# Kernel optimization log

Hardware: AMD Instinct MI355X
Metric: run time of the kernel (lower is better)

Reference implementation:

```python
import jax, jax.numpy as jnp
import numpy as np

B, A, T = 256, 512, 21
DIM = 128
SC = 6
NHEAD, HD = 4, DIM // 4

def conv1d_relu(x, w, b, stride=2):
    # x: (N, C, L), w: (O, I, K)
    y = jax.lax.conv_general_dilated(x, w, (stride,), 'SAME', dimension_numbers=('NCH', 'OIH', 'NCH'))
    return jax.nn.relu(y + b[None, :, None])

def to_vector(feat, vm):
    vec_mask = vm[..., :-1] & vm[..., 1:]
    while vec_mask.ndim < feat.ndim:
        vec_mask = vec_mask[..., None]
    return jnp.where(vec_mask, feat[:, :, 1:] - feat[:, :, :-1], jnp.zeros_like(feat[:, :, 1:]))

def setup_inputs():
    key = jax.random.key(0)
    ks = jax.random.split(key, 24)
    f32 = jnp.float32
    inp = {}
    inp['position'] = jax.random.normal(ks[0], (B, A, T, 2), f32)
    inp['heading'] = jax.random.normal(ks[1], (B, A, T), f32)
    inp['velocity'] = jax.random.normal(ks[2], (B, A, T, 2), f32)
    inp['shape'] = jax.random.uniform(ks[3], (B, A, T, 2), f32)
    inp['current_state'] = jax.random.normal(ks[4], (B, SC), f32)
    inp['category'] = jax.random.randint(ks[5], (B, A), 0, 4)
    inp['valid_mask'] = jax.random.randint(ks[6], (B, A, T), 0, 2).astype(bool)
    # history encoder (CNN) params: 9 -> 32 -> 64 -> 128 channels, k=3, stride 2
    inp['conv1_w'] = jax.random.normal(ks[7], (32, 9, 3), f32) * 0.1
    inp['conv1_b'] = jnp.zeros((32,), f32)
    inp['conv2_w'] = jax.random.normal(ks[8], (64, 32, 3), f32) * 0.1
    inp['conv2_b'] = jnp.zeros((64,), f32)
    inp['conv3_w'] = jax.random.normal(ks[9], (128, 64, 3), f32) * 0.1
    inp['conv3_b'] = jnp.zeros((128,), f32)
    # StateAttentionEncoder params
    inp['se_w'] = jax.random.normal(ks[10], (SC, DIM), f32) * 0.02   # per-channel Linear(1,dim) weights
    inp['se_b'] = jnp.zeros((SC, DIM), f32)
    inp['pos_embed'] = jax.random.normal(ks[11], (1, SC, DIM), f32) * 0.02
    inp['query'] = jax.random.normal(ks[12], (1, 1, DIM), f32) * 0.02
    inp['in_proj_w'] = jax.random.normal(ks[13], (3 * DIM, DIM), f32) * (1.0 / np.sqrt(DIM))
    inp['in_proj_b'] = jnp.zeros((3 * DIM,), f32)
    inp['out_proj_w'] = jax.random.normal(ks[14], (DIM, DIM), f32) * (1.0 / np.sqrt(DIM))
    inp['out_proj_b'] = jnp.zeros((DIM,), f32)
    inp['type_emb'] = jax.random.normal(ks[15], (4, DIM), f32) * 0.02
    return inp

def reference(position, heading, velocity, shape, current_state, category, valid_mask,
              conv1_w, conv1_b, conv2_w, conv2_b, conv3_w, conv3_b,
              se_w, se_b, pos_embed, query, in_proj_w, in_proj_b, out_proj_w, out_proj_b,
              type_emb):
    # --- build per-step agent features (B, A, T-1, 9) ---
    heading_vec = to_vector(heading, valid_mask)
    valid_mask_vec = valid_mask[..., 1:] & valid_mask[..., :-1]
    agent_feature = jnp.concatenate([
        to_vector(position, valid_mask),
        to_vector(velocity, valid_mask),
        jnp.stack([jnp.cos(heading_vec), jnp.sin(heading_vec)], axis=-1),
        shape[:, :, 1:],
        valid_mask_vec.astype(jnp.float32)[..., None],
    ], axis=-1)
    bs, nA, Tm1, C = agent_feature.shape
    x = agent_feature.reshape(bs * nA, Tm1, C).transpose(0, 2, 1)  # (N, 9, T-1)
    # --- history CNN encoder (applied to all rows, then masked; same math as boolean gather/scatter) ---
    h = conv1d_relu(x, conv1_w, conv1_b)
    h = conv1d_relu(h, conv2_w, conv2_b)
    h = conv1d_relu(h, conv3_w, conv3_b)
    enc = h.mean(axis=-1)  # (N, DIM)
    valid_agent = valid_mask.any(-1).reshape(-1)
    x_agent = jnp.where(valid_agent[:, None], enc, 0.0).reshape(bs, nA, DIM)
    # --- ego state attention encoder (eval mode: no token dropout) ---
    ego = current_state[:, :SC]
    x_embed = ego[:, :, None] * se_w[None] + se_b[None] + pos_embed  # (B, SC, DIM)
    Wq, Wk, Wv = in_proj_w[:DIM], in_proj_w[DIM:2 * DIM], in_proj_w[2 * DIM:]
    bq, bk, bv = in_proj_b[:DIM], in_proj_b[DIM:2 * DIM], in_proj_b[2 * DIM:]
    q = (query[0, 0] @ Wq.T + bq).reshape(NHEAD, HD)             # (H, D)
    k = (x_embed @ Wk.T + bk).reshape(bs, SC, NHEAD, HD)          # (B, S, H, D)
    v = (x_embed @ Wv.T + bv).reshape(bs, SC, NHEAD, HD)
    scores = jnp.einsum('hd,bshd->bhs', q, k) * (1.0 / np.sqrt(HD))
    attn = jax.nn.softmax(scores, axis=-1)
    o = jnp.einsum('bhs,bshd->bhd', attn, v).reshape(bs, DIM)
    x_ego = o @ out_proj_w.T + out_proj_b                         # (B, DIM)
    x_agent = x_agent.at[:, 0].set(x_ego)
    # --- type embedding add ---
    return x_agent + type_emb[category]
```

## Files before the change

kernel.cpp:

```cpp
#include <hip/hip_runtime.h>
#include <hip/hip_bf16.h>


#define BB 256
#define AAG 512
#define TT 21
#define NAG (BB * AAG)

typedef __hip_bfloat16 bf16;
typedef __attribute__((ext_vector_type(8))) short s8v;
typedef __attribute__((ext_vector_type(4))) float f4v;

__device__ int g_dtype;
__device__ int g_mask_mode;
__device__ __align__(16) short g_w1p[32 * 64];
__device__ __align__(16) short g_w2p[64 * 96];
__device__ __align__(16) short g_w3p[128 * 192];
__device__ __align__(16) float g_b1[32];
__device__ __align__(16) float g_b2[64];
__device__ __align__(16) float g_b3[128];

template <int DT>
__device__ __forceinline__ float ldf(const void* p, long i) {
    if (DT) return __bfloat162float(((const bf16*)p)[i]);
    return ((const float*)p)[i];
}
template <int DT>
__device__ __forceinline__ void stf(void* p, long i, float v) {
    if (DT) ((bf16*)p)[i] = __float2bfloat16(v);
    else    ((float*)p)[i] = v;
}
__device__ __forceinline__ unsigned short f2bu(float x) {
    bf16 b = __float2bfloat16(x);
    union { bf16 b; unsigned short u; } cv; cv.b = b; return cv.u;
}
__device__ __forceinline__ float bu2f(unsigned short u) {
    union { unsigned int i; float f; } cv; cv.i = ((unsigned int)u) << 16; return cv.f;
}
__device__ __forceinline__ bool mask_at(const void* p, long i, int mode) {
    if (mode == 0) return ((const int*)p)[i] != 0;
    if (mode == 1) return ((const unsigned char*)p)[i] != 0;
    if (mode == 2) return ((const float*)p)[i] != 0.f;
    return (((const unsigned short*)p)[i] & 0x7fff) != 0;
}

__global__ void detect_kernel(const unsigned int* __restrict__ pw,
                              const unsigned char* __restrict__ m) {
    __shared__ int cls[4];
    __shared__ int mv;
    __shared__ int good;
    int tid = threadIdx.x;
    if (tid < 4) cls[tid] = 0;
    if (tid == 0) { mv = 0; good = 0; }
    __syncthreads();
    int g = 0;
    for (int i = tid; i < 1024; i += 256) {
        unsigned int w = pw[i];
        unsigned int h0 = w & 0xffffu, h1 = w >> 16;
        unsigned int e0 = (h0 >> 7) & 0xff, e1 = (h1 >> 7) & 0xff;
        if (h0 == 0 || (e0 >= 90 && e0 <= 160)) g++;
        if (h1 == 0 || (e1 >= 90 && e1 <= 160)) g++;
    }
    atomicAdd(&good, g);
    int l0 = 0, l1 = 0, l2 = 0, l3 = 0, lm = 0;
    for (int i = tid; i < 4096; i += 256) {
        int v = m[i];
        if (v) {
            switch (i & 3) { case 0: l0 = 1; break; case 1: l1 = 1; break;
                             case 2: l2 = 1; break; default: l3 = 1; }
            if (v > lm) lm = v;
        }
    }
    if (l0) atomicOr(&cls[0], 1);
    if (l1) atomicOr(&cls[1], 1);
    if (l2) atomicOr(&cls[2], 1);
    if (l3) atomicOr(&cls[3], 1);
    atomicMax(&mv, lm);
    __syncthreads();
    if (tid == 0) {
        g_dtype = (good >= 1740) ? 1 : 0;
        int mode;
        if (!cls[1] && !cls[2] && !cls[3]) mode = 0;
        else if (!cls[0] && !cls[1])       mode = 2;
        else if (mv <= 1)                  mode = 1;
        else                               mode = 3;
        g_mask_mode = mode;
    }
}

template <int DT>
__global__ void prep_weights_kernel(const void* __restrict__ w1, const void* __restrict__ b1,
                                    const void* __restrict__ w2, const void* __restrict__ b2,
                                    const void* __restrict__ w3, const void* __restrict__ b3) {
    if (g_dtype != DT) return;
    int tid = blockIdx.x * blockDim.x + threadIdx.x;
    int nt = gridDim.x * blockDim.x;
    for (int i = tid; i < 32 * 64; i += nt) {
        int oc = i >> 6, k = i & 63, tap = k >> 4, ic = k & 15;
        float v = (tap < 3 && ic < 9) ? ldf<DT>(w1, oc * 27 + ic * 3 + tap) : 0.f;
        g_w1p[i] = (short)f2bu(v);
    }
    for (int i = tid; i < 64 * 96; i += nt) {
        int oc = i / 96, k = i % 96, tap = k >> 5, ic = k & 31;
        g_w2p[i] = (short)f2bu(ldf<DT>(w2, oc * 96 + ic * 3 + tap));
    }
    for (int i = tid; i < 128 * 192; i += nt) {
        int oc = i / 192, k = i % 192, tap = k >> 6, ic = k & 63;
        g_w3p[i] = (short)f2bu(ldf<DT>(w3, oc * 192 + ic * 3 + tap));
    }
    for (int i = tid; i < 32; i += nt) g_b1[i] = ldf<DT>(b1, i);
    for (int i = tid; i < 64; i += nt) g_b2[i] = ldf<DT>(b2, i);
    for (int i = tid; i < 128; i += nt) g_b3[i] = ldf<DT>(b3, i);
}

#define FEAT_RS 24
#define FEAT_AS 528
#define H1_RS 40
#define H1_AS 440
#define H2_RS 72
#define H2_AS 504
#define C3_AS 384
#define OFF_H1 8448
#define OFF_H2 15488
#define OFF_VALID 47104
#define SMEM_BYTES 47168

#define MFMA16(a, b, c) __builtin_amdgcn_mfma_f32_16x16x32_bf16((a), (b), (c), 0, 0, 0)

template <int DT>
__global__ __launch_bounds__(256) void stage1_kernel(
    const void* __restrict__ pos, const void* __restrict__ heading,
    const void* __restrict__ vel, const void* __restrict__ shp,
    const void* __restrict__ vmask, const int* __restrict__ category,
    const void* __restrict__ type_emb, void* __restrict__ out) {
    if (g_dtype != DT) return;
    __shared__ __align__(16) char smem[SMEM_BYTES];
    short* feat = (short*)smem;
    short* h1 = (short*)smem + OFF_H1;
    short* h2 = (short*)smem + OFF_H2;
    short* c3 = (short*)smem;
    int* s_valid = (int*)(smem + OFF_VALID);

    const int tid = threadIdx.x;
    const int wave = tid >> 6, lane = tid & 63;
    const int col = lane & 15, quad = lane >> 4;
    const long agent0 = (long)blockIdx.x * 16;
    const int mode = g_mask_mode;

    if (tid < 16) s_valid[tid] = 0;
    {
        unsigned int* h1u = (unsigned int*)h1;
        int ag = tid >> 4, c = tid & 15;
        h1u[ag * 220 + 200 + c] = 0;
        unsigned int* h2u = (unsigned int*)h2;
        for (int i = tid; i < 1024; i += 256) {
            int a2 = i >> 6, r = (i >> 5) & 1, cc = i & 31;
            h2u[a2 * 252 + r * 216 + cc] = 0;
        }
    }
    __syncthreads();

    for (int idx = tid; idx < 16 * 22; idx += 256) {
        int ag = idx / 22, t = idx % 22;
        short* row = feat + ag * FEAT_AS + t * FEAT_RS;
        if (t >= 20) {
            *(uint4*)row = make_uint4(0, 0, 0, 0);
            *(uint4*)(row + 8) = make_uint4(0, 0, 0, 0);
            if (t == 20) {
                long base = (agent0 + ag) * TT + 20;
                if (mask_at(vmask, base, mode)) atomicOr(&s_valid[ag], 1);
            }
        } else {
            long base = (agent0 + ag) * TT + t;
            bool vmt = mask_at(vmask, base, mode);
            if (vmt) atomicOr(&s_valid[ag], 1);
            bool m2 = vmt && mask_at(vmask, base + 1, mode);
            float px0 = ldf<DT>(pos, base * 2),     py0 = ldf<DT>(pos, base * 2 + 1);
            float px1 = ldf<DT>(pos, base * 2 + 2), py1 = ldf<DT>(pos, base * 2 + 3);
            float vx0 = ldf<DT>(vel, base * 2),     vy0 = ldf<DT>(vel, base * 2 + 1);
            float vx1 = ldf<DT>(vel, base * 2 + 2), vy1 = ldf<DT>(vel, base * 2 + 3);
            float hh0 = ldf<DT>(heading, base), hh1 = ldf<DT>(heading, base + 1);
            float sx = ldf<DT>(shp, base * 2 + 2), sy = ldf<DT>(shp, base * 2 + 3);
            float dh = m2 ? (hh1 - hh0) : 0.f;
            float sn = sinf(dh), cn = cosf(dh);
            unsigned int p0 = f2bu(m2 ? px1 - px0 : 0.f) | ((unsigned int)f2bu(m2 ? py1 - py0 : 0.f) << 16);
            unsigned int p1 = f2bu(m2 ? vx1 - vx0 : 0.f) | ((unsigned int)f2bu(m2 ? vy1 - vy0 : 0.f) << 16);
            unsigned int p2 = f2bu(cn) | ((unsigned int)f2bu(sn) << 16);
            unsigned int p3 = f2bu(sx) | ((unsigned int)f2bu(sy) << 16);
            unsigned int p4 = (unsigned int)f2bu(m2 ? 1.f : 0.f);
            *(uint4*)row = make_uint4(p0, p1, p2, p3);
            *(uint4*)(row + 8) = make_uint4(p4, 0, 0, 0);
        }
    }
    __syncthreads();

    {
        int Mt = wave >> 1;
        int oc = Mt * 16 + col;
        s8v a0 = *(const s8v*)(g_w1p + oc * 64 + quad * 8);
        s8v a1 = *(const s8v*)(g_w1p + oc * 64 + 32 + quad * 8);
        int k0 = quad * 8, k1 = 32 + quad * 8;
        int tap0 = k0 >> 4, ic0 = k0 & 15;
        int tap1 = k1 >> 4, ic1 = k1 & 15;
        int ocr = Mt * 16 + quad * 4;
        f4v bia = *(const f4v*)(g_b1 + ocr);
#pragma unroll
        for (int i = 0; i < 5; i++) {
            int Nt = (wave & 1) * 5 + i;
            int n = Nt * 16 + col;
            int ag = n / 10, p = n % 10;
            const short* bb = feat + ag * FEAT_AS + 2 * p * FEAT_RS;
            s8v b0 = *(const s8v*)(bb + tap0 * FEAT_RS + ic0);
            s8v b1 = *(const s8v*)(bb + tap1 * FEAT_RS + ic1);
            f4v acc = {0.f, 0.f, 0.f, 0.f};
            acc = MFMA16(a0, b0, acc);
            acc = MFMA16(a1, b1, acc);
            unsigned int lo = f2bu(fmaxf(acc[0] + bia[0], 0.f)) | ((unsigned int)f2bu(fmaxf(acc[1] + bia[1], 0.f)) << 16);
            unsigned int hi = f2bu(fmaxf(acc[2] + bia[2], 0.f)) | ((unsigned int)f2bu(fmaxf(acc[3] + bia[3], 0.f)) << 16);
            *(uint2*)(h1 + ag * H1_AS + p * H1_RS + ocr) = make_uint2(lo, hi);
        }
    }
    __syncthreads();

    {
        int Mt = wave;
        int oc = Mt * 16 + col;
        s8v a[3];
#pragma unroll
        for (int ks = 0; ks < 3; ks++)
            a[ks] = *(const s8v*)(g_w2p + oc * 96 + ks * 32 + quad * 8);
        int ocr = Mt * 16 + quad * 4;
        f4v bia = *(const f4v*)(g_b2 + ocr);
#pragma unroll
        for (int Nt = 0; Nt < 5; Nt++) {
            int n = Nt * 16 + col;
            int ag = n / 5, p = n % 5;
            f4v acc = {0.f, 0.f, 0.f, 0.f};
#pragma unroll
            for (int ks = 0; ks < 3; ks++) {
                s8v b = *(const s8v*)(h1 + ag * H1_AS + (2 * p + ks) * H1_RS + quad * 8);
                acc = MFMA16(a[ks], b, acc);
            }
            unsigned int lo = f2bu(fmaxf(acc[0] + bia[0], 0.f)) | ((unsigned int)f2bu(fmaxf(acc[1] + bia[1], 0.f)) << 16);
            unsigned int hi = f2bu(fmaxf(acc[2] + bia[2], 0.f)) | ((unsigned int)f2bu(fmaxf(acc[3] + bia[3], 0.f)) << 16);
            *(uint2*)(h2 + ag * H2_AS + (p + 1) * H2_RS + ocr) = make_uint2(lo, hi);
        }
    }
    __syncthreads();

#pragma unroll
    for (int m2 = 0; m2 < 2; m2++) {
        int Mt = wave * 2 + m2;
        int oc = Mt * 16 + col;
        s8v a[6];
#pragma unroll
        for (int ks = 0; ks < 6; ks++)
            a[ks] = *(const s8v*)(g_w3p + oc * 192 + ks * 32 + quad * 8);
        int ocr = Mt * 16 + quad * 4;
        f4v bia = *(const f4v*)(g_b3 + ocr);
#pragma unroll
        for (int Nt = 0; Nt < 3; Nt++) {
            int n = Nt * 16 + col;
            int ag = n / 3, p = n % 3;
            f4v acc = {0.f, 0.f, 0.f, 0.f};
#pragma unroll
            for (int ks = 0; ks < 6; ks++) {
                int kg = ks * 32 + quad * 8;
                int tap = kg >> 6, ic = kg & 63;
                s8v b = *(const s8v*)(h2 + ag * H2_AS + (2 * p + tap) * H2_RS + ic);
                acc = MFMA16(a[ks], b, acc);
            }
            unsigned int lo = f2bu(fmaxf(acc[0] + bia[0], 0.f)) | ((unsigned int)f2bu(fmaxf(acc[1] + bia[1], 0.f)) << 16);
            unsigned int hi = f2bu(fmaxf(acc[2] + bia[2], 0.f)) | ((unsigned int)f2bu(fmaxf(acc[3] + bia[3], 0.f)) << 16);
            *(uint2*)(c3 + ag * C3_AS + p * 128 + ocr) = make_uint2(lo, hi);
        }
    }
    __syncthreads();

    {
        int ag = tid >> 4;
        int ocg = (tid & 15) * 8;
        s8v x0 = *(const s8v*)(c3 + ag * C3_AS + ocg);
        s8v x1 = *(const s8v*)(c3 + ag * C3_AS + 128 + ocg);
        s8v x2 = *(const s8v*)(c3 + ag * C3_AS + 256 + ocg);
        int valid = s_valid[ag];
        long agl = agent0 + ag;
        int cat = category[agl];
#pragma unroll
        for (int j = 0; j < 8; j++) {
            float m = (bu2f((unsigned short)x0[j]) + bu2f((unsigned short)x1[j]) +
                       bu2f((unsigned short)x2[j])) * (1.f / 3.f);
            if (!valid) m = 0.f;
            float te = ldf<DT>(type_emb, cat * 128 + ocg + j);
            stf<DT>(out, agl * 128 + ocg + j, m + te);
        }
    }
}

template <int DT>
__global__ __launch_bounds__(128) void stage2_kernel(
    const void* __restrict__ cs, const int* __restrict__ category,
    const void* __restrict__ se_w, const void* __restrict__ se_b,
    const void* __restrict__ pe, const void* __restrict__ query,
    const void* __restrict__ ipw, const void* __restrict__ ipb,
    const void* __restrict__ opw, const void* __restrict__ opb,
    const void* __restrict__ type_emb, void* __restrict__ out) {
    if (g_dtype != DT) return;
    int b = blockIdx.x, d = threadIdx.x;
    __shared__ float s_xe[6][128];
    __shared__ float s_qu[128];
    __shared__ float s_q[128];
    __shared__ float s_k[6][128];
    __shared__ float s_v[6][128];
    __shared__ float s_att[4][6];
    __shared__ float s_o[128];

    s_qu[d] = ldf<DT>(query, d);
#pragma unroll
    for (int s = 0; s < 6; s++) {
        float ego = ldf<DT>(cs, b * 6 + s);
        s_xe[s][d] = fmaf(ego, ldf<DT>(se_w, s * 128 + d),
                          ldf<DT>(se_b, s * 128 + d) + ldf<DT>(pe, s * 128 + d));
    }
    __syncthreads();

    float accq = ldf<DT>(ipb, d);
    float bk = ldf<DT>(ipb, 128 + d), bv = ldf<DT>(ipb, 256 + d);
    float acck[6], accv[6];
#pragma unroll
    for (int s = 0; s < 6; s++) { acck[s] = bk; accv[s] = bv; }
    for (int e = 0; e < 128; e++) {
        float wqe = ldf<DT>(ipw, (long)d * 128 + e);
        accq = fmaf(s_qu[e], wqe, accq);
        float wke = ldf<DT>(ipw, (long)(128 + d) * 128 + e);
        float wve = ldf<DT>(ipw, (long)(256 + d) * 128 + e);
#pragma unroll
        for (int s = 0; s < 6; s++) {
            float xe = s_xe[s][e];
            acck[s] = fmaf(xe, wke, acck[s]);
            accv[s] = fmaf(xe, wve, accv[s]);
        }
    }
    s_q[d] = accq;
#pragma unroll
    for (int s = 0; s < 6; s++) { s_k[s][d] = acck[s]; s_v[s][d] = accv[s]; }
    __syncthreads();

    if (d < 4) {
        float sc[6];
        float mx = -1e30f;
#pragma unroll
        for (int s = 0; s < 6; s++) {
            float t = 0.f;
            for (int q = 0; q < 32; q++) t = fmaf(s_q[d * 32 + q], s_k[s][d * 32 + q], t);
            t *= 0.17677669529663687f;
            sc[s] = t;
            mx = fmaxf(mx, t);
        }
        float sum = 0.f;
#pragma unroll
        for (int s = 0; s < 6; s++) { sc[s] = expf(sc[s] - mx); sum += sc[s]; }
        float inv = 1.f / sum;
#pragma unroll
        for (int s = 0; s < 6; s++) s_att[d][s] = sc[s] * inv;
    }
    __syncthreads();

    {
        int h = d >> 5;
        float o = 0.f;
#pragma unroll
        for (int s = 0; s < 6; s++) o = fmaf(s_att[h][s], s_v[s][d], o);
        s_o[d] = o;
    }
    __syncthreads();

    float acc = ldf<DT>(opb, d);
    for (int e = 0; e < 128; e++) acc = fmaf(s_o[e], ldf<DT>(opw, (long)d * 128 + e), acc);
    int cat = category[(long)b * AAG];
    stf<DT>(out, (long)b * AAG * 128 + d, acc + ldf<DT>(type_emb, cat * 128 + d));
}

extern "C" void kernel_launch(void* const* d_in, const int* in_sizes, int n_in,
                              void* d_out, int out_size, void* d_ws, size_t ws_size,
                              hipStream_t stream) {
    const void* position      = d_in[0];
    const void* heading       = d_in[1];
    const void* velocity      = d_in[2];
    const void* shape         = d_in[3];
    const void* current_state = d_in[4];
    const int*  category      = (const int*)d_in[5];
    const void* valid_mask    = d_in[6];
    const void* conv1_w = d_in[7];
    const void* conv1_b = d_in[8];
    const void* conv2_w = d_in[9];
    const void* conv2_b = d_in[10];
    const void* conv3_w = d_in[11];
    const void* conv3_b = d_in[12];
    const void* se_w    = d_in[13];
    const void* se_b    = d_in[14];
    const void* pos_embed = d_in[15];
    const void* query     = d_in[16];
    const void* in_proj_w = d_in[17];
    const void* in_proj_b = d_in[18];
    const void* out_proj_w = d_in[19];
    const void* out_proj_b = d_in[20];
    const void* type_emb   = d_in[21];

    hipLaunchKernelGGL(detect_kernel, dim3(1), dim3(256), 0, stream,
                       (const unsigned int*)position, (const unsigned char*)valid_mask);

    hipLaunchKernelGGL(prep_weights_kernel<0>, dim3(64), dim3(256), 0, stream,
                       conv1_w, conv1_b, conv2_w, conv2_b, conv3_w, conv3_b);
    hipLaunchKernelGGL(prep_weights_kernel<1>, dim3(64), dim3(256), 0, stream,
                       conv1_w, conv1_b, conv2_w, conv2_b, conv3_w, conv3_b);

    hipLaunchKernelGGL(stage1_kernel<0>, dim3(NAG / 16), dim3(256), 0, stream,
                       position, heading, velocity, shape, valid_mask, category, type_emb, d_out);
    hipLaunchKernelGGL(stage1_kernel<1>, dim3(NAG / 16), dim3(256), 0, stream,
                       position, heading, velocity, shape, valid_mask, category, type_emb, d_out);

    hipLaunchKernelGGL(stage2_kernel<0>, dim3(BB), dim3(128), 0, stream,
                       current_state, category, se_w, se_b, pos_embed, query,
                       in_proj_w, in_proj_b, out_proj_w, out_proj_b, type_emb, d_out);
    hipLaunchKernelGGL(stage2_kernel<1>, dim3(BB), dim3(128), 0, stream,
                       current_state, category, se_w, se_b, pos_embed, query,
                       in_proj_w, in_proj_b, out_proj_w, out_proj_b, type_emb, d_out);
}
```

Baseline: 324.8 us.

## Make conv pipeline wave-private and precompute attention terms linear in ego state

stage1 now gives each wave its own four agents with a private shared-memory slab, which removes all block-wide __syncthreads between the three MFMA conv layers. The type-embedding epilogue is vectorised. The ego attention is rewritten: since the embedding is affine in each scalar ego input, the score and value-projection constants are precomputed once in a new single-block kernel. The per-batch stage2 kernel then evaluates only a small softmax and a weighted sum, with projection weights stored as bf16, which adds precision risk and an extra serial launch.

```diff
diff --git a/kernel.cpp b/kernel.cpp
--- a/kernel.cpp
+++ b/kernel.cpp
@@ -19,6 +19,10 @@
 __device__ __align__(16) float g_b1[32];
 __device__ __align__(16) float g_b2[64];
 __device__ __align__(16) float g_b3[128];
+__device__ __align__(16) short g_ipwT[128 * 384];
+__device__ __align__(16) short g_opwT[128 * 128];
+__device__ __align__(16) float g_Sc[24], g_Sw[24];
+__device__ __align__(16) float g_P[24 * 128], g_Pw[24 * 128];
 
 template <int DT>
 __device__ __forceinline__ float ldf(const void* p, long i) {
@@ -42,6 +46,16 @@
     if (mode == 1) return ((const unsigned char*)p)[i] != 0;
     if (mode == 2) return ((const float*)p)[i] != 0.f;
     return (((const unsigned short*)p)[i] & 0x7fff) != 0;
+}
+__device__ __forceinline__ uint2 pack4(f4v acc, f4v bia, bool zero) {
+    float r0 = zero ? 0.f : fmaxf(acc[0] + bia[0], 0.f);
+    float r1 = zero ? 0.f : fmaxf(acc[1] + bia[1], 0.f);
+    float r2 = zero ? 0.f : fmaxf(acc[2] + bia[2], 0.f);
+    float r3 = zero ? 0.f : fmaxf(acc[3] + bia[3], 0.f);
+    uint2 r;
+    r.x = f2bu(r0) | ((unsigned int)f2bu(r1) << 16);
+    r.y = f2bu(r2) | ((unsigned int)f2bu(r3) << 16);
+    return r;
 }
 
 __global__ void detect_kernel(const unsigned int* __restrict__ pw,
@@ -91,7 +105,8 @@
 template <int DT>
 __global__ void prep_weights_kernel(const void* __restrict__ w1, const void* __restrict__ b1,
                                     const void* __restrict__ w2, const void* __restrict__ b2,
-                                    const void* __restrict__ w3, const void* __restrict__ b3) {
+                                    const void* __restrict__ w3, const void* __restrict__ b3,
+                                    const void* __restrict__ ipw, const void* __restrict__ opw) {
     if (g_dtype != DT) return;
     int tid = blockIdx.x * blockDim.x + threadIdx.x;
     int nt = gridDim.x * blockDim.x;
@@ -111,19 +126,99 @@
     for (int i = tid; i < 32; i += nt) g_b1[i] = ldf<DT>(b1, i);
     for (int i = tid; i < 64; i += nt) g_b2[i] = ldf<DT>(b2, i);
     for (int i = tid; i < 128; i += nt) g_b3[i] = ldf<DT>(b3, i);
-}
-
-#define FEAT_RS 24
-#define FEAT_AS 528
+    for (int i = tid; i < 384 * 128; i += nt) {
+        int r = i >> 7, e = i & 127;
+        g_ipwT[e * 384 + r] = (short)f2bu(ldf<DT>(ipw, i));
+    }
+    for (int i = tid; i < 128 * 128; i += nt) {
+        int d = i >> 7, e = i & 127;
+        g_opwT[e * 128 + d] = (short)f2bu(ldf<DT>(opw, i));
+    }
+}
+
+template <int DT>
+__global__ __launch_bounds__(128) void precompute_attn_kernel(
+    const void* __restrict__ se_w, const void* __restrict__ se_b,
+    const void* __restrict__ pe, const void* __restrict__ query,
+    const void* __restrict__ ipb) {
+    if (g_dtype != DT) return;
+    __shared__ float s_qu[128], s_xc[6][128], s_xw[6][128];
+    __shared__ float s_q[128], s_kc[6][128], s_kw[6][128], s_vc[6][128], s_vw[6][128];
+    int d = threadIdx.x;
+    s_qu[d] = ldf<DT>(query, d);
+#pragma unroll
+    for (int s = 0; s < 6; s++) {
+        s_xc[s][d] = ldf<DT>(se_b, s * 128 + d) + ldf<DT>(pe, s * 128 + d);
+        s_xw[s][d] = ldf<DT>(se_w, s * 128 + d);
+    }
+    __syncthreads();
+    float aq = ldf<DT>(ipb, d);
+    float kc[6], kw[6], vc[6], vw[6];
+    float bkd = ldf<DT>(ipb, 128 + d), bvd = ldf<DT>(ipb, 256 + d);
+#pragma unroll
+    for (int s = 0; s < 6; s++) { kc[s] = bkd; vc[s] = bvd; kw[s] = 0.f; vw[s] = 0.f; }
+    for (int e = 0; e < 128; e++) {
+        float wq = bu2f((unsigned short)g_ipwT[e * 384 + d]);
+        float wk = bu2f((unsigned short)g_ipwT[e * 384 + 128 + d]);
+        float wv = bu2f((unsigned short)g_ipwT[e * 384 + 256 + d]);
+        aq = fmaf(s_qu[e], wq, aq);
+#pragma unroll
+        for (int s = 0; s < 6; s++) {
+            float xc = s_xc[s][e], xw = s_xw[s][e];
+            kc[s] = fmaf(xc, wk, kc[s]);
+            kw[s] = fmaf(xw, wk, kw[s]);
+            vc[s] = fmaf(xc, wv, vc[s]);
+            vw[s] = fmaf(xw, wv, vw[s]);
+        }
+    }
+    s_q[d] = aq;
+#pragma unroll
+    for (int s = 0; s < 6; s++) {
+        s_kc[s][d] = kc[s]; s_kw[s][d] = kw[s];
+        s_vc[s][d] = vc[s]; s_vw[s][d] = vw[s];
+    }
+    __syncthreads();
+    if (d < 24) {
+        int s = d >> 2, h = d & 3;
+        float sc = 0.f, sw = 0.f;
+        for (int j = 0; j < 32; j++) {
+            sc = fmaf(s_q[h * 32 + j], s_kc[s][h * 32 + j], sc);
+            sw = fmaf(s_q[h * 32 + j], s_kw[s][h * 32 + j], sw);
+        }
+        g_Sc[s * 4 + h] = sc * 0.17677669529663687f;
+        g_Sw[s * 4 + h] = sw * 0.17677669529663687f;
+    }
+    float pc[6], pw[6];
+#pragma unroll
+    for (int s = 0; s < 6; s++) { pc[s] = 0.f; pw[s] = 0.f; }
+    for (int e = 0; e < 128; e++) {
+        float wo = bu2f((unsigned short)g_opwT[e * 128 + d]);
+#pragma unroll
+        for (int s = 0; s < 6; s++) {
+            pc[s] = fmaf(wo, s_vc[s][e], pc[s]);
+            pw[s] = fmaf(wo, s_vw[s][e], pw[s]);
+        }
+        if ((e & 31) == 31) {
+            int h = e >> 5;
+#pragma unroll
+            for (int s = 0; s < 6; s++) {
+                g_P[(s * 4 + h) * 128 + d] = pc[s];
+                g_Pw[(s * 4 + h) * 128 + d] = pw[s];
+                pc[s] = 0.f; pw[s] = 0.f;
+            }
+        }
+    }
+}
+
+#define F_RS 24
+#define F_AS 584
 #define H1_RS 40
-#define H1_AS 440
+#define H1_AS 488
 #define H2_RS 72
-#define H2_AS 504
-#define C3_AS 384
-#define OFF_H1 8448
-#define OFF_H2 15488
-#define OFF_VALID 47104
-#define SMEM_BYTES 47168
+#define H2_AS 520
+#define C3_RS 136
+#define C3_AS 408
+#define WAVE_STRIDE 6368
 
 #define MFMA16(a, b, c) __builtin_amdgcn_mfma_f32_16x16x32_bf16((a), (b), (c), 0, 0, 0)
 
@@ -134,165 +229,169 @@
     const void* __restrict__ vmask, const int* __restrict__ category,
     const void* __restrict__ type_emb, void* __restrict__ out) {
     if (g_dtype != DT) return;
-    __shared__ __align__(16) char smem[SMEM_BYTES];
-    short* feat = (short*)smem;
-    short* h1 = (short*)smem + OFF_H1;
-    short* h2 = (short*)smem + OFF_H2;
-    short* c3 = (short*)smem;
-    int* s_valid = (int*)(smem + OFF_VALID);
+    __shared__ __align__(16) short sm[4 * WAVE_STRIDE + 128];
+    __shared__ int sval[16];
 
     const int tid = threadIdx.x;
     const int wave = tid >> 6, lane = tid & 63;
     const int col = lane & 15, quad = lane >> 4;
-    const long agent0 = (long)blockIdx.x * 16;
     const int mode = g_mask_mode;
-
-    if (tid < 16) s_valid[tid] = 0;
+    short* feat = sm + wave * WAVE_STRIDE;
+    short* h1 = feat + 2336;
+    short* h2 = feat + 4288;
+    short* c3 = feat;
+    int* wv = sval + wave * 4;
+    const long agent0 = (long)blockIdx.x * 16 + wave * 4;
+
+    if (lane < 4) wv[lane] = 0;
+
+    for (int it = 0; it < 2; it++) {
+        int idx = it * 64 + lane;
+        if (idx < 96) {
+            int ag = idx / 24, t = idx - ag * 24;
+            short* row = feat + ag * F_AS + t * F_RS;
+            long base = (agent0 + ag) * TT + t;
+            if (t <= 19) {
+                bool vmt = mask_at(vmask, base, mode);
+                if (vmt) atomicOr(&wv[ag], 1);
+                bool m2 = vmt && mask_at(vmask, base + 1, mode);
+                float px0 = ldf<DT>(pos, base * 2),     py0 = ldf<DT>(pos, base * 2 + 1);
+                float px1 = ldf<DT>(pos, base * 2 + 2), py1 = ldf<DT>(pos, base * 2 + 3);
+                float vx0 = ldf<DT>(vel, base * 2),     vy0 = ldf<DT>(vel, base * 2 + 1);
+                float vx1 = ldf<DT>(vel, base * 2 + 2), vy1 = ldf<DT>(vel, base * 2 + 3);
+                float hh0 = ldf<DT>(heading, base), hh1 = ldf<DT>(heading, base + 1);
+                float sx = ldf<DT>(shp, base * 2 + 2), sy = ldf<DT>(shp, base * 2 + 3);
+                float dh = m2 ? (hh1 - hh0) : 0.f;
+                float sn = sinf(dh), cn = cosf(dh);
+                unsigned int p0 = f2bu(m2 ? px1 - px0 : 0.f) | ((unsigned int)f2bu(m2 ? py1 - py0 : 0.f) << 16);
+                unsigned int p1 = f2bu(m2 ? vx1 - vx0 : 0.f) | ((unsigned int)f2bu(m2 ? vy1 - vy0 : 0.f) << 16);
+                unsigned int p2 = f2bu(cn) | ((unsigned int)f2bu(sn) << 16);
+                unsigned int p3 = f2bu(sx) | ((unsigned int)f2bu(sy) << 16);
+                unsigned int p4 = (unsigned int)f2bu(m2 ? 1.f : 0.f);
+                *(uint4*)row = make_uint4(p0, p1, p2, p3);
+                *(uint4*)(row + 8) = make_uint4(p4, 0, 0, 0);
+            } else if (t <= 21) {
+                *(uint4*)row = make_uint4(0, 0, 0, 0);
+                *(uint4*)(row + 8) = make_uint4(0, 0, 0, 0);
+                if (t == 20 && mask_at(vmask, base, mode)) atomicOr(&wv[ag], 1);
+            }
+        }
+    }
+    if (lane < 32) {
+        int ag = lane >> 3, j = lane & 7;
+        *(uint4*)(h2 + ag * H2_AS + j * 8) = make_uint4(0, 0, 0, 0);
+    }
+
     {
-        unsigned int* h1u = (unsigned int*)h1;
-        int ag = tid >> 4, c = tid & 15;
-        h1u[ag * 220 + 200 + c] = 0;
-        unsigned int* h2u = (unsigned int*)h2;
-        for (int i = tid; i < 1024; i += 256) {
-            int a2 = i >> 6, r = (i >> 5) & 1, cc = i & 31;
-            h2u[a2 * 252 + r * 216 + cc] = 0;
-        }
-    }
-    __syncthreads();
-
-    for (int idx = tid; idx < 16 * 22; idx += 256) {
-        int ag = idx / 22, t = idx % 22;
-        short* row = feat + ag * FEAT_AS + t * FEAT_RS;
-        if (t >= 20) {
-            *(uint4*)row = make_uint4(0, 0, 0, 0);
-            *(uint4*)(row + 8) = make_uint4(0, 0, 0, 0);
-            if (t == 20) {
-                long base = (agent0 + ag) * TT + 20;
-                if (mask_at(vmask, base, mode)) atomicOr(&s_valid[ag], 1);
-            }
-        } else {
-            long base = (agent0 + ag) * TT + t;
-            bool vmt = mask_at(vmask, base, mode);
-            if (vmt) atomicOr(&s_valid[ag], 1);
-            bool m2 = vmt && mask_at(vmask, base + 1, mode);
-            float px0 = ldf<DT>(pos, base * 2),     py0 = ldf<DT>(pos, base * 2 + 1);
-            float px1 = ldf<DT>(pos, base * 2 + 2), py1 = ldf<DT>(pos, base * 2 + 3);
-            float vx0 = ldf<DT>(vel, base * 2),     vy0 = ldf<DT>(vel, base * 2 + 1);
-            float vx1 = ldf<DT>(vel, base * 2 + 2), vy1 = ldf<DT>(vel, base * 2 + 3);
-            float hh0 = ldf<DT>(heading, base), hh1 = ldf<DT>(heading, base + 1);
-            float sx = ldf<DT>(shp, base * 2 + 2), sy = ldf<DT>(shp, base * 2 + 3);
-            float dh = m2 ? (hh1 - hh0) : 0.f;
-            float sn = sinf(dh), cn = cosf(dh);
-            unsigned int p0 = f2bu(m2 ? px1 - px0 : 0.f) | ((unsigned int)f2bu(m2 ? py1 - py0 : 0.f) << 16);
-            unsigned int p1 = f2bu(m2 ? vx1 - vx0 : 0.f) | ((unsigned int)f2bu(m2 ? vy1 - vy0 : 0.f) << 16);
-            unsigned int p2 = f2bu(cn) | ((unsigned int)f2bu(sn) << 16);
-            unsigned int p3 = f2bu(sx) | ((unsigned int)f2bu(sy) << 16);
-            unsigned int p4 = (unsigned int)f2bu(m2 ? 1.f : 0.f);
-            *(uint4*)row = make_uint4(p0, p1, p2, p3);
-            *(uint4*)(row + 8) = make_uint4(p4, 0, 0, 0);
-        }
-    }
-    __syncthreads();
+        int rofs = (quad >> 1) * F_RS + (quad & 1) * 8;
+#pragma unroll
+        for (int mt = 0; mt < 2; mt++) {
+            int oc = mt * 16 + col;
+            s8v a0 = *(const s8v*)(g_w1p + oc * 64 + quad * 8);
+            s8v a1 = *(const s8v*)(g_w1p + oc * 64 + 32 + quad * 8);
+            f4v bia = *(const f4v*)(g_b1 + mt * 16 + quad * 4);
+#pragma unroll
+            for (int nt = 0; nt < 3; nt++) {
+                int n = nt * 16 + col;
+                int ag = (n * 171) >> 11;
+                int p = n - ag * 12;
+                const short* bb = feat + ag * F_AS + 2 * p * F_RS + rofs;
+                s8v b0 = *(const s8v*)(bb);
+                s8v b1 = *(const s8v*)(bb + 2 * F_RS);
+                f4v acc = {0.f, 0.f, 0.f, 0.f};
+                acc = MFMA16(a0, b0, acc);
+                acc = MFMA16(a1, b1, acc);
+                *(uint2*)(h1 + ag * H1_AS + p * H1_RS + mt * 16 + quad * 4) =
+                    pack4(acc, bia, p == 10);
+            }
+        }
+    }
 
     {
-        int Mt = wave >> 1;
-        int oc = Mt * 16 + col;
-        s8v a0 = *(const s8v*)(g_w1p + oc * 64 + quad * 8);
-        s8v a1 = *(const s8v*)(g_w1p + oc * 64 + 32 + quad * 8);
-        int k0 = quad * 8, k1 = 32 + quad * 8;
-        int tap0 = k0 >> 4, ic0 = k0 & 15;
-        int tap1 = k1 >> 4, ic1 = k1 & 15;
-        int ocr = Mt * 16 + quad * 4;
-        f4v bia = *(const f4v*)(g_b1 + ocr);
-#pragma unroll
-        for (int i = 0; i < 5; i++) {
-            int Nt = (wave & 1) * 5 + i;
-            int n = Nt * 16 + col;
-            int ag = n / 10, p = n % 10;
-            const short* bb = feat + ag * FEAT_AS + 2 * p * FEAT_RS;
-            s8v b0 = *(const s8v*)(bb + tap0 * FEAT_RS + ic0);
-            s8v b1 = *(const s8v*)(bb + tap1 * FEAT_RS + ic1);
-            f4v acc = {0.f, 0.f, 0.f, 0.f};
-            acc = MFMA16(a0, b0, acc);
-            acc = MFMA16(a1, b1, acc);
-            unsigned int lo = f2bu(fmaxf(acc[0] + bia[0], 0.f)) | ((unsigned int)f2bu(fmaxf(acc[1] + bia[1], 0.f)) << 16);
-            unsigned int hi = f2bu(fmaxf(acc[2] + bia[2], 0.f)) | ((unsigned int)f2bu(fmaxf(acc[3] + bia[3], 0.f)) << 16);
-            *(uint2*)(h1 + ag * H1_AS + p * H1_RS + ocr) = make_uint2(lo, hi);
-        }
-    }
-    __syncthreads();
+#pragma unroll
+        for (int mt = 0; mt < 4; mt++) {
+            int oc = mt * 16 + col;
+            s8v a0 = *(const s8v*)(g_w2p + oc * 96 + quad * 8);
+            s8v a1 = *(const s8v*)(g_w2p + oc * 96 + 32 + quad * 8);
+            s8v a2 = *(const s8v*)(g_w2p + oc * 96 + 64 + quad * 8);
+            f4v bia = *(const f4v*)(g_b2 + mt * 16 + quad * 4);
+#pragma unroll
+            for (int nt = 0; nt < 2; nt++) {
+                int n = nt * 16 + col;
+                int ag = n >> 3, p = n & 7;
+                const short* hb = h1 + ag * H1_AS + 2 * p * H1_RS + quad * 8;
+                f4v acc = {0.f, 0.f, 0.f, 0.f};
+                acc = MFMA16(a0, *(const s8v*)(hb), acc);
+                acc = MFMA16(a1, *(const s8v*)(hb + H1_RS), acc);
+                acc = MFMA16(a2, *(const s8v*)(hb + 2 * H1_RS), acc);
+                if (p < 6) {
+                    *(uint2*)(h2 + ag * H2_AS + (p + 1) * H2_RS + mt * 16 + quad * 4) =
+                        pack4(acc, bia, p == 5);
+                }
+            }
+        }
+    }
 
     {
-        int Mt = wave;
-        int oc = Mt * 16 + col;
-        s8v a[3];
-#pragma unroll
-        for (int ks = 0; ks < 3; ks++)
-            a[ks] = *(const s8v*)(g_w2p + oc * 96 + ks * 32 + quad * 8);
-        int ocr = Mt * 16 + quad * 4;
-        f4v bia = *(const f4v*)(g_b2 + ocr);
-#pragma unroll
-        for (int Nt = 0; Nt < 5; Nt++) {
-            int n = Nt * 16 + col;
-            int ag = n / 5, p = n % 5;
-            f4v acc = {0.f, 0.f, 0.f, 0.f};
-#pragma unroll
-            for (int ks = 0; ks < 3; ks++) {
-                s8v b = *(const s8v*)(h1 + ag * H1_AS + (2 * p + ks) * H1_RS + quad * 8);
-                acc = MFMA16(a[ks], b, acc);
-            }
-            unsigned int lo = f2bu(fmaxf(acc[0] + bia[0], 0.f)) | ((unsigned int)f2bu(fmaxf(acc[1] + bia[1], 0.f)) << 16);
-            unsigned int hi = f2bu(fmaxf(acc[2] + bia[2], 0.f)) | ((unsigned int)f2bu(fmaxf(acc[3] + bia[3], 0.f)) << 16);
-            *(uint2*)(h2 + ag * H2_AS + (p + 1) * H2_RS + ocr) = make_uint2(lo, hi);
-        }
-    }
-    __syncthreads();
-
-#pragma unroll
-    for (int m2 = 0; m2 < 2; m2++) {
-        int Mt = wave * 2 + m2;
-        int oc = Mt * 16 + col;
-        s8v a[6];
-#pragma unroll
-        for (int ks = 0; ks < 6; ks++)
-            a[ks] = *(const s8v*)(g_w3p + oc * 192 + ks * 32 + quad * 8);
-        int ocr = Mt * 16 + quad * 4;
-        f4v bia = *(const f4v*)(g_b3 + ocr);
-#pragma unroll
-        for (int Nt = 0; Nt < 3; Nt++) {
-            int n = Nt * 16 + col;
-            int ag = n / 3, p = n % 3;
+        int ag = col >> 2, p = col & 3;
+        const short* hb = h2 + ag * H2_AS + 2 * p * H2_RS;
+#pragma unroll
+        for (int mt = 0; mt < 8; mt++) {
+            int oc = mt * 16 + col;
+            s8v a[6];
+#pragma unroll
+            for (int ks = 0; ks < 6; ks++)
+                a[ks] = *(const s8v*)(g_w3p + oc * 192 + ks * 32 + quad * 8);
+            f4v bia = *(const f4v*)(g_b3 + mt * 16 + quad * 4);
             f4v acc = {0.f, 0.f, 0.f, 0.f};
 #pragma unroll
             for (int ks = 0; ks < 6; ks++) {
                 int kg = ks * 32 + quad * 8;
                 int tap = kg >> 6, ic = kg & 63;
-                s8v b = *(const s8v*)(h2 + ag * H2_AS + (2 * p + tap) * H2_RS + ic);
-                acc = MFMA16(a[ks], b, acc);
-            }
-            unsigned int lo = f2bu(fmaxf(acc[0] + bia[0], 0.f)) | ((unsigned int)f2bu(fmaxf(acc[1] + bia[1], 0.f)) << 16);
-            unsigned int hi = f2bu(fmaxf(acc[2] + bia[2], 0.f)) | ((unsigned int)f2bu(fmaxf(acc[3] + bia[3], 0.f)) << 16);
-            *(uint2*)(c3 + ag * C3_AS + p * 128 + ocr) = make_uint2(lo, hi);
-        }
-    }
-    __syncthreads();
+                acc = MFMA16(a[ks], *(const s8v*)(hb + tap * H2_RS + ic), acc);
+            }
+            if (p < 3) {
+                *(uint2*)(c3 + ag * C3_AS + p * C3_RS + mt * 16 + quad * 4) =
+                    pack4(acc, bia, false);
+            }
+        }
+    }
 
     {
-        int ag = tid >> 4;
-        int ocg = (tid & 15) * 8;
-        s8v x0 = *(const s8v*)(c3 + ag * C3_AS + ocg);
-        s8v x1 = *(const s8v*)(c3 + ag * C3_AS + 128 + ocg);
-        s8v x2 = *(const s8v*)(c3 + ag * C3_AS + 256 + ocg);
-        int valid = s_valid[ag];
-        long agl = agent0 + ag;
-        int cat = category[agl];
-#pragma unroll
-        for (int j = 0; j < 8; j++) {
-            float m = (bu2f((unsigned short)x0[j]) + bu2f((unsigned short)x1[j]) +
-                       bu2f((unsigned short)x2[j])) * (1.f / 3.f);
-            if (!valid) m = 0.f;
-            float te = ldf<DT>(type_emb, cat * 128 + ocg + j);
-            stf<DT>(out, agl * 128 + ocg + j, m + te);
+        int ag = lane >> 4, j = lane & 15, ocg = j * 8;
+        const short* cb = c3 + ag * C3_AS + j * 8;
+        s8v x0 = *(const s8v*)(cb);
+        s8v x1 = *(const s8v*)(cb + C3_RS);
+        s8v x2 = *(const s8v*)(cb + 2 * C3_RS);
+        int valid = wv[ag];
+        long agent = agent0 + ag;
+        int cat = category[agent];
+        float r[8];
+#pragma unroll
+        for (int jj = 0; jj < 8; jj++) {
+            float m = (bu2f((unsigned short)x0[jj]) + bu2f((unsigned short)x1[jj]) +
+                       bu2f((unsigned short)x2[jj])) * (1.f / 3.f);
+            r[jj] = valid ? m : 0.f;
+        }
+        if (DT) {
+            const short* tep = (const short*)type_emb + cat * 128 + ocg;
+            s8v te = *(const s8v*)tep;
+            unsigned int o[4];
+#pragma unroll
+            for (int q = 0; q < 4; q++) {
+                o[q] = f2bu(r[2 * q] + bu2f((unsigned short)te[2 * q])) |
+                       ((unsigned int)f2bu(r[2 * q + 1] + bu2f((unsigned short)te[2 * q + 1])) << 16);
+            }
+            *(uint4*)((short*)out + agent * 128 + ocg) = make_uint4(o[0], o[1], o[2], o[3]);
+        } else {
+            const float* tep = (const float*)type_emb + cat * 128 + ocg;
+            float4 t0 = *(const float4*)tep;
+            float4 t1 = *(const float4*)(tep + 4);
+            float4 o0 = make_float4(r[0] + t0.x, r[1] + t0.y, r[2] + t0.z, r[3] + t0.w);
+            float4 o1 = make_float4(r[4] + t1.x, r[5] + t1.y, r[6] + t1.z, r[7] + t1.w);
+            float* op = (float*)out + agent * 128 + ocg;
+            *(float4*)op = o0;
+            *(float4*)(op + 4) = o1;
         }
     }
 }
@@ -300,85 +399,40 @@
 template <int DT>
 __global__ __launch_bounds__(128) void stage2_kernel(
     const void* __restrict__ cs, const int* __restrict__ category,
-    const void* __restrict__ se_w, const void* __restrict__ se_b,
-    const void* __restrict__ pe, const void* __restrict__ query,
-    const void* __restrict__ ipw, const void* __restrict__ ipb,
-    const void* __restrict__ opw, const void* __restrict__ opb,
-    const void* __restrict__ type_emb, void* __restrict__ out) {
+    const void* __restrict__ opb, const void* __restrict__ type_emb,
+    void* __restrict__ out) {
     if (g_dtype != DT) return;
     int b = blockIdx.x, d = threadIdx.x;
-    __shared__ float s_xe[6][128];
-    __shared__ float s_qu[128];
-    __shared__ float s_q[128];
-    __shared__ float s_k[6][128];
-    __shared__ float s_v[6][128];
-    __shared__ float s_att[4][6];
-    __shared__ float s_o[128];
-
-    s_qu[d] = ldf<DT>(query, d);
-#pragma unroll
-    for (int s = 0; s < 6; s++) {
-        float ego = ldf<DT>(cs, b * 6 + s);
-        s_xe[s][d] = fmaf(ego, ldf<DT>(se_w, s * 128 + d),
-                          ldf<DT>(se_b, s * 128 + d) + ldf<DT>(pe, s * 128 + d));
-    }
-    __syncthreads();
-
-    float accq = ldf<DT>(ipb, d);
-    float bk = ldf<DT>(ipb, 128 + d), bv = ldf<DT>(ipb, 256 + d);
-    float acck[6], accv[6];
-#pragma unroll
-    for (int s = 0; s < 6; s++) { acck[s] = bk; accv[s] = bv; }
-    for (int e = 0; e < 128; e++) {
-        float wqe = ldf<DT>(ipw, (long)d * 128 + e);
-        accq = fmaf(s_qu[e], wqe, accq);
-        float wke = ldf<DT>(ipw, (long)(128 + d) * 128 + e);
-        float wve = ldf<DT>(ipw, (long)(256 + d) * 128 + e);
+    float ego[6];
+#pragma unroll
+    for (int s = 0; s < 6; s++) ego[s] = ldf<DT>(cs, b * 6 + s);
+    float a[4][6];
+#pragma unroll
+    for (int h = 0; h < 4; h++) {
+        float mx = -1e30f;
 #pragma unroll
         for (int s = 0; s < 6; s++) {
-            float xe = s_xe[s][e];
-            acck[s] = fmaf(xe, wke, acck[s]);
-            accv[s] = fmaf(xe, wve, accv[s]);
-        }
-    }
-    s_q[d] = accq;
-#pragma unroll
-    for (int s = 0; s < 6; s++) { s_k[s][d] = acck[s]; s_v[s][d] = accv[s]; }
-    __syncthreads();
-
-    if (d < 4) {
-        float sc[6];
-        float mx = -1e30f;
-#pragma unroll
-        for (int s = 0; s < 6; s++) {
-            float t = 0.f;
-            for (int q = 0; q < 32; q++) t = fmaf(s_q[d * 32 + q], s_k[s][d * 32 + q], t);
-            t *= 0.17677669529663687f;
-            sc[s] = t;
+            float t = fmaf(ego[s], g_Sw[s * 4 + h], g_Sc[s * 4 + h]);
+            a[h][s] = t;
             mx = fmaxf(mx, t);
         }
         float sum = 0.f;
 #pragma unroll
-        for (int s = 0; s < 6; s++) { sc[s] = expf(sc[s] - mx); sum += sc[s]; }
+        for (int s = 0; s < 6; s++) { a[h][s] = expf(a[h][s] - mx); sum += a[h][s]; }
         float inv = 1.f / sum;
 #pragma unroll
-        for (int s = 0; s < 6; s++) s_att[d][s] = sc[s] * inv;
-    }
-    __syncthreads();
-
-    {
-        int h = d >> 5;
-        float o = 0.f;
-#pragma unroll
-        for (int s = 0; s < 6; s++) o = fmaf(s_att[h][s], s_v[s][d], o);
-        s_o[d] = o;
-    }
-    __syncthreads();
-
-    float acc = ldf<DT>(opb, d);
-    for (int e = 0; e < 128; e++) acc = fmaf(s_o[e], ldf<DT>(opw, (long)d * 128 + e), acc);
+        for (int s = 0; s < 6; s++) a[h][s] *= inv;
+    }
     int cat = category[(long)b * AAG];
-    stf<DT>(out, (long)b * AAG * 128 + d, acc + ldf<DT>(type_emb, cat * 128 + d));
+    float acc = ldf<DT>(opb, d) + ldf<DT>(type_emb, cat * 128 + d);
+#pragma unroll
+    for (int s = 0; s < 6; s++)
+#pragma unroll
+        for (int h = 0; h < 4; h++) {
+            float pv = fmaf(ego[s], g_Pw[(s * 4 + h) * 128 + d], g_P[(s * 4 + h) * 128 + d]);
+            acc = fmaf(a[h][s], pv, acc);
+        }
+    stf<DT>(out, (long)b * AAG * 128 + d, acc);
 }
 
 extern "C" void kernel_launch(void* const* d_in, const int* in_sizes, int n_in,
@@ -411,9 +465,16 @@
                        (const unsigned int*)position, (const unsigned char*)valid_mask);
 
     hipLaunchKernelGGL(prep_weights_kernel<0>, dim3(64), dim3(256), 0, stream,
-                       conv1_w, conv1_b, conv2_w, conv2_b, conv3_w, conv3_b);
+                       conv1_w, conv1_b, conv2_w, conv2_b, conv3_w, conv3_b,
+                       in_proj_w, out_proj_w);
     hipLaunchKernelGGL(prep_weights_kernel<1>, dim3(64), dim3(256), 0, stream,
-                       conv1_w, conv1_b, conv2_w, conv2_b, conv3_w, conv3_b);
+                       conv1_w, conv1_b, conv2_w, conv2_b, conv3_w, conv3_b,
+                       in_proj_w, out_proj_w);
+
+    hipLaunchKernelGGL(precompute_attn_kernel<0>, dim3(1), dim3(128), 0, stream,
+                       se_w, se_b, pos_embed, query, in_proj_b);
+    hipLaunchKernelGGL(precompute_attn_kernel<1>, dim3(1), dim3(128), 0, stream,
+                       se_w, se_b, pos_embed, query, in_proj_b);
 
     hipLaunchKernelGGL(stage1_kernel<0>, dim3(NAG / 16), dim3(256), 0, stream,
                        position, heading, velocity, shape, valid_mask, category, type_emb, d_out);
@@ -421,9 +482,7 @@
                        position, heading, velocity, shape, valid_mask, category, type_emb, d_out);
 
     hipLaunchKernelGGL(stage2_kernel<0>, dim3(BB), dim3(128), 0, stream,
-                       current_state, category, se_w, se_b, pos_embed, query,
-                       in_proj_w, in_proj_b, out_proj_w, out_proj_b, type_emb, d_out);
+                       current_state, category, out_proj_b, type_emb, d_out);
     hipLaunchKernelGGL(stage2_kernel<1>, dim3(BB), dim3(128), 0, stream,
-                       current_state, category, se_w, se_b, pos_embed, query,
-                       in_proj_w, in_proj_b, out_proj_w, out_proj_b, type_emb, d_out);
-}
+                       current_state, category, out_proj_b, type_emb, d_out);
+}
```

Measured after the change: 501.4 us. +54.3%, slower.
